# Performance work log

Hardware: AMD Instinct MI355X
Metric: run time of the kernel (lower is better)

Reference implementation:

```python
import jax, jax.numpy as jnp
import numpy as np

NUM_HEADS = 8
EMBED_CH = 512   # k channels
OUT_CH = 256     # v channels
MASK_CURRENT = False
NEG_INF = -1e30


def setup_inputs() -> dict:
    key = jax.random.key(0)
    ks = jax.random.split(key, 7)
    N, C, H, W = 8, 256, 32, 32
    s = lambda fan: 1.0 / np.sqrt(fan)
    return {
        "x": jax.random.normal(ks[0], (N, C, H, W), jnp.float32),
        "Wq": jax.random.normal(ks[1], (EMBED_CH, C), jnp.float32) * s(C),
        "bq": jax.random.normal(ks[2], (EMBED_CH,), jnp.float32) * 0.01,
        "Wkv": jax.random.normal(ks[3], (EMBED_CH + OUT_CH, C), jnp.float32) * s(C),
        "bkv": jax.random.normal(ks[4], (EMBED_CH + OUT_CH,), jnp.float32) * 0.01,
        "Wo": jax.random.normal(ks[5], (OUT_CH, OUT_CH), jnp.float32) * s(OUT_CH),
        "bo": jax.random.normal(ks[6], (OUT_CH,), jnp.float32) * 0.01,
    }


def _to_multihead(t, n, T):
    # t: [n, h*d, T] with channel layout '(h d)' -> [n, h, T, d]
    h = NUM_HEADS
    return t.reshape(n, h, -1, T).transpose(0, 1, 3, 2)


def reference(x, Wq, bq, Wkv, bkv, Wo, bo):
    n, C, H, W = x.shape
    T = H * W
    xf = x.reshape(n, C, T)  # flatten spatial dims into sequence

    # 1x1 convs == pointwise channel GEMMs
    q = jnp.einsum('oc,nct->not', Wq, xf) + bq[None, :, None]
    kv = jnp.einsum('oc,nct->not', Wkv, xf) + bkv[None, :, None]
    k, v = kv[:, :EMBED_CH], kv[:, EMBED_CH:]

    q = _to_multihead(q, n, T)   # [n, h, T, dk]
    k = _to_multihead(k, n, T)   # [n, h, T, dk]
    v = _to_multihead(v, n, T)   # [n, h, T, dv]

    dk = k.shape[-1]
    scale = 1.0 / np.sqrt(dk).astype(np.float32)

    # causal mask over flattened spatial positions (lower-triangular)
    diag = -1 if MASK_CURRENT else 0
    mask = jnp.tril(jnp.ones((T, T), dtype=bool), k=diag)  # [T, T]

    attn = jnp.einsum('nhtd,nhsd->nhts', q, k) * scale
    attn = jnp.where(mask[None, None], attn, NEG_INF)
    attn = jax.nn.softmax(attn, axis=-1)
    attn = jnp.where(mask[None, None], attn, 0.0)

    out = jnp.einsum('nhts,nhsd->nhtd', attn, v)            # [n, h, T, dv]
    out = out.transpose(0, 1, 3, 2).reshape(n, OUT_CH, T)   # n (h d) t

    out = jnp.einsum('oc,nct->not', Wo, out) + bo[None, :, None]
    return out.reshape(n, OUT_CH, H, W)
```

## Files before the change

kernel.cpp:

```cpp
#include <hip/hip_runtime.h>
#include <hip/hip_bf16.h>
#include <math.h>

typedef __bf16 bf16;
typedef __attribute__((ext_vector_type(4))) __bf16 bf16x4;
typedef __attribute__((ext_vector_type(8))) __bf16 bf16x8;
typedef __attribute__((ext_vector_type(4))) float f32x4;

#define T_DIM 1024
#define C_DIM 256
#define HEADS 8

static __device__ __forceinline__ int tb(int row, int col) {
  return row * 128 + ((((col >> 3) ^ row) & 7) << 4) + ((col & 7) << 1);
}

static __device__ __forceinline__ void gl16(const char* g, char* l) {
  __builtin_amdgcn_global_load_lds(
      (const __attribute__((address_space(1))) unsigned int*)g,
      (__attribute__((address_space(3))) unsigned int*)l, 16, 0, 0);
}
static __device__ __forceinline__ void stage16k(const char* g, char* l, int tid) {
  const int w = (tid >> 6) * 1024, ln = (tid & 63) * 16;
#pragma unroll
  for (int i = 0; i < 4; ++i) gl16(g + i * 4096 + w + ln, l + i * 4096 + w);
}
static __device__ __forceinline__ void stage8k(const char* g, char* l, int tid) {
  const int w = (tid >> 6) * 1024, ln = (tid & 63) * 16;
#pragma unroll
  for (int i = 0; i < 2; ++i) gl16(g + i * 4096 + w + ln, l + i * 4096 + w);
}
static __device__ __forceinline__ void stage4k(const char* g, char* l, int tid) {
  gl16(g + (tid >> 6) * 1024 + (tid & 63) * 16, l + (tid >> 6) * 1024);
}

__global__ __launch_bounds__(256) void k_prep(const float* __restrict__ x,
    const float* __restrict__ Wq, const float* __restrict__ Wkv, const float* __restrict__ Wo,
    char* __restrict__ xTt, char* __restrict__ Wbt, char* __restrict__ Wot) {
  const int tid = threadIdx.x;
  const int b = blockIdx.x;
  if (b < 512) {
    __shared__ float tile[64][65];
    const int n = b >> 6, rem = b & 63, tt64 = rem >> 2, ct = (rem & 3) << 6;
    const float* xp = x + ((size_t)n * C_DIM + ct) * T_DIM + tt64 * 64;
    const int t4 = (tid & 15) * 4, c0 = tid >> 4;
#pragma unroll
    for (int i = 0; i < 4; ++i) {
      const int c = c0 + i * 16;
      float4 v = *(const float4*)(xp + (size_t)c * T_DIM + t4);
      tile[c][t4] = v.x; tile[c][t4 + 1] = v.y; tile[c][t4 + 2] = v.z; tile[c][t4 + 3] = v.w;
    }
    __syncthreads();
    char* dst = xTt + (((size_t)(n * 8 + (tt64 >> 1))) * 4 + (rem & 3)) * 16384;
    const int rbase = (tt64 & 1) * 64;
#pragma unroll
    for (int i = 0; i < 2; ++i) {
      const int idx = tid + i * 256;
      const int tl = idx >> 3, c8 = (idx & 7) * 8;
      bf16x8 v;
#pragma unroll
      for (int j = 0; j < 8; ++j) v[j] = (bf16)tile[c8 + j][tl];
      *(bf16x8*)(dst + tb(rbase + tl, c8)) = v;
    }
  } else {
    const bool isWo = (b >= 532);
    const int o0 = (b - (isWo ? 532 : 512)) * 64;
#pragma unroll
    for (int i = 0; i < 8; ++i) {
      const int idx = tid + i * 256;
      const int row = idx >> 5, c8 = (idx & 31) * 8;
      const int o = o0 + row;
      const float* src = isWo ? (Wo + (size_t)o * C_DIM + c8)
                              : (o < 512 ? Wq + (size_t)o * C_DIM + c8
                                         : Wkv + (size_t)(o - 512) * C_DIM + c8);
      float4 a = *(const float4*)src;
      float4 bq4 = *(const float4*)(src + 4);
      bf16x8 v;
      v[0]=(bf16)a.x; v[1]=(bf16)a.y; v[2]=(bf16)a.z; v[3]=(bf16)a.w;
      v[4]=(bf16)bq4.x; v[5]=(bf16)bq4.y; v[6]=(bf16)bq4.z; v[7]=(bf16)bq4.w;
      char* base = isWo ? Wot : Wbt;
      char* dst = base + (((size_t)(o >> 7)) * 4 + (c8 >> 6)) * 16384;
      *(bf16x8*)(dst + tb(o & 127, c8 & 63)) = v;
    }
  }
}

__global__ __launch_bounds__(256) void k_qkv(const char* __restrict__ Wbt, const char* __restrict__ xTt,
    const float* __restrict__ bq, const float* __restrict__ bkv,
    bf16* __restrict__ q_ws, char* __restrict__ Kt, char* __restrict__ Vt) {
  __shared__ __attribute__((aligned(128))) unsigned char smem[34816];
  const int tid = threadIdx.x;
  const int nt = blockIdx.x, mt = blockIdx.y, n = blockIdx.z;
  const int w = tid >> 6, lane = tid & 63, lrow = lane & 15, lg = lane >> 4;
  const int wm = (w >> 1) * 64, wn = (w & 1) * 64;
  const char* gA = Wbt + (size_t)mt * 65536;
  const char* gB = xTt + ((size_t)(n * 8 + nt)) * 65536;

  f32x4 acc[4][4] = {};
#pragma unroll 1
  for (int kk = 0; kk < 4; ++kk) {
    stage16k(gA + kk * 16384, (char*)smem, tid);
    stage16k(gB + kk * 16384, (char*)smem + 16384, tid);
    __syncthreads();
    const char* As = (const char*)smem;
    const char* Bs = As + 16384;
    bf16x8 af[4][2], bv[4][2];
#pragma unroll
    for (int mi = 0; mi < 4; ++mi)
#pragma unroll
      for (int kh = 0; kh < 2; ++kh)
        af[mi][kh] = *(const bf16x8*)(As + tb(wm + mi * 16 + lrow, kh * 32 + lg * 8));
#pragma unroll
    for (int ni = 0; ni < 4; ++ni)
#pragma unroll
      for (int kh = 0; kh < 2; ++kh)
        bv[ni][kh] = *(const bf16x8*)(Bs + tb(wn + ni * 16 + lrow, kh * 32 + lg * 8));
#pragma unroll
    for (int kh = 0; kh < 2; ++kh)
#pragma unroll
      for (int mi = 0; mi < 4; ++mi)
#pragma unroll
        for (int ni = 0; ni < 4; ++ni)
          acc[mi][ni] = __builtin_amdgcn_mfma_f32_16x16x32_bf16(af[mi][kh], bv[ni][kh], acc[mi][ni], 0, 0, 0);
    __syncthreads();
  }

  const int obase = mt * 128 + wm + lg * 4;
  const int tcol0 = nt * 128 + wn + lrow;
  if (mt < 8) {
#pragma unroll
    for (int mi = 0; mi < 4; ++mi) {
      const int o = obase + mi * 16;
      if (mt < 4) {
        const float4 bb = *(const float4*)(bq + o);
        const int nh = n * 8 + (o >> 6), d = o & 63;
        bf16* qrow = q_ws + (size_t)nh * (T_DIM * 64) + d;
#pragma unroll
        for (int ni = 0; ni < 4; ++ni) {
          const int t = tcol0 + ni * 16;
          f32x4 v = acc[mi][ni];
          bf16x4 pk;
          pk[0]=(bf16)(v[0]+bb.x); pk[1]=(bf16)(v[1]+bb.y); pk[2]=(bf16)(v[2]+bb.z); pk[3]=(bf16)(v[3]+bb.w);
          *(bf16x4*)(qrow + (size_t)t * 64) = pk;
        }
      } else {
        const int o2 = o - 512;
        const float4 bb = *(const float4*)(bkv + o2);
        const int nh = n * 8 + (o2 >> 6), d = o2 & 63;
        char* tbase = Kt + (size_t)nh * 16 * 8192;
#pragma unroll
        for (int ni = 0; ni < 4; ++ni) {
          const int t = tcol0 + ni * 16;
          f32x4 v = acc[mi][ni];
          bf16x4 pk;
          pk[0]=(bf16)(v[0]+bb.x); pk[1]=(bf16)(v[1]+bb.y); pk[2]=(bf16)(v[2]+bb.z); pk[3]=(bf16)(v[3]+bb.w);
          *(bf16x4*)(tbase + (t >> 6) * 8192 + tb(t & 63, d)) = pk;
        }
      }
    }
  } else {
    bf16* tp = (bf16*)smem;
#pragma unroll
    for (int mi = 0; mi < 4; ++mi) {
      const int o3g = (mt - 8) * 128 + wm + mi * 16 + lg * 4;
      const float4 bb = *(const float4*)(bkv + 512 + o3g);
      const float* bbp = (const float*)&bb;
      const int o3l = wm + mi * 16 + lg * 4;
#pragma unroll
      for (int ni = 0; ni < 4; ++ni) {
        const int tl = wn + ni * 16 + lrow;
        f32x4 v = acc[mi][ni];
#pragma unroll
        for (int r = 0; r < 4; ++r)
          tp[(o3l + r) * 132 + tl] = (bf16)(v[r] + bbp[r]);
      }
    }
    __syncthreads();
    const int row = tid >> 1, half = tid & 1;
    const int o3 = (mt - 8) * 128 + row;
    const int nh = n * 8 + (o3 >> 5), dv = o3 & 31;
    char* tile = Vt + (size_t)nh * 16 * 4096 + (nt * 2 + half) * 4096;
    const bf16* src = tp + row * 132 + half * 64;
#pragma unroll
    for (int g = 0; g < 8; ++g) {
      bf16x4 lo = *(const bf16x4*)(src + g * 8);
      bf16x4 hi = *(const bf16x4*)(src + g * 8 + 4);
      bf16x8 vv;
      vv[0]=lo[0]; vv[1]=lo[1]; vv[2]=lo[2]; vv[3]=lo[3];
      vv[4]=hi[0]; vv[5]=hi[1]; vv[6]=hi[2]; vv[7]=hi[3];
      *(bf16x8*)(tile + tb(dv, g * 8)) = vv;
    }
  }
}

__global__ __launch_bounds__(256) void k_attn(const bf16* __restrict__ q_ws,
    const char* __restrict__ Kt, const char* __restrict__ Vt, char* __restrict__ attTt) {
  __shared__ __attribute__((aligned(128))) unsigned char smem[40960];
  const int tid = threadIdx.x;
  const int nh = blockIdx.x, qp = blockIdx.y;
  const int w = tid >> 6, lane = tid & 63, lrow = lane & 15, lg = lane >> 4;
  const int tl = w * 16 + lrow;
  const char* Ktb = Kt + (size_t)nh * 16 * 8192;
  const char* Vtb = Vt + (size_t)nh * 16 * 4096;
  const int n = nh >> 3, h = nh & 7;
  const float s2 = 0.18033688f;

  const int qt0 = qp, qt1 = 15 - qp;
  const int tg0 = qt0 * 64 + tl, tg1 = qt1 * 64 + tl;
  const bf16* qb0 = q_ws + ((size_t)nh * T_DIM + tg0) * 64;
  const bf16* qb1 = q_ws + ((size_t)nh * T_DIM + tg1) * 64;
  const bf16x8 qA0 = *(const bf16x8*)(qb0 + lg * 8);
  const bf16x8 qA1 = *(const bf16x8*)(qb0 + 32 + lg * 8);
  const bf16x8 qB0 = *(const bf16x8*)(qb1 + lg * 8);
  const bf16x8 qB1 = *(const bf16x8*)(qb1 + 32 + lg * 8);

  float m0 = -INFINITY, l0 = 0.f, m1 = -INFINITY, l1 = 0.f;
  f32x4 o0a = {}, o0b = {}, o1a = {}, o1b = {};

  auto proc = [&](bf16x8 qf0, bf16x8 qf1, float& m, float& l, f32x4& oa, f32x4& ob,
                  const char* Kbs, const char* Vbs, char* pws, bool diag) {
    f32x4 sacc[4];
    __builtin_amdgcn_s_setprio(1);
#pragma unroll
    for (int rt = 0; rt < 4; ++rt) {
      f32x4 a = {0.f, 0.f, 0.f, 0.f};
      bf16x8 kf0 = *(const bf16x8*)(Kbs + tb(rt * 16 + lrow, lg * 8));
      a = __builtin_amdgcn_mfma_f32_16x16x32_bf16(kf0, qf0, a, 0, 0, 0);
      bf16x8 kf1 = *(const bf16x8*)(Kbs + tb(rt * 16 + lrow, 32 + lg * 8));
      a = __builtin_amdgcn_mfma_f32_16x16x32_bf16(kf1, qf1, a, 0, 0, 0);
      sacc[rt] = a;
    }
    __builtin_amdgcn_s_setprio(0);
    float p[16];
#pragma unroll
    for (int rt = 0; rt < 4; ++rt)
#pragma unroll
      for (int r = 0; r < 4; ++r) {
        float v = sacc[rt][r] * s2;
        if (diag && (rt * 16 + lg * 4 + r) > tl) v = -INFINITY;
        p[rt * 4 + r] = v;
      }
    float pmax = p[0];
#pragma unroll
    for (int i = 1; i < 16; ++i) pmax = fmaxf(pmax, p[i]);
    pmax = fmaxf(pmax, __shfl_xor(pmax, 16));
    pmax = fmaxf(pmax, __shfl_xor(pmax, 32));
    const float mn = fmaxf(m, pmax);
    const float corr = exp2f(m - mn);
    float ps = 0.f;
#pragma unroll
    for (int i = 0; i < 16; ++i) { p[i] = exp2f(p[i] - mn); ps += p[i]; }
    ps += __shfl_xor(ps, 16);
    ps += __shfl_xor(ps, 32);
    l = l * corr + ps;
    m = mn;
    oa = oa * corr;
    ob = ob * corr;
#pragma unroll
    for (int rt = 0; rt < 4; ++rt) {
      bf16x4 pk;
#pragma unroll
      for (int r = 0; r < 4; ++r) pk[r] = (bf16)p[rt * 4 + r];
      *(bf16x4*)(pws + tb(lrow, rt * 16 + lg * 4)) = pk;
    }
    __builtin_amdgcn_s_setprio(1);
#pragma unroll
    for (int ks = 0; ks < 2; ++ks) {
      bf16x8 pf = *(const bf16x8*)(pws + tb(lrow, ks * 32 + lg * 8));
      bf16x8 vf0 = *(const bf16x8*)(Vbs + tb(lrow, ks * 32 + lg * 8));
      oa = __builtin_amdgcn_mfma_f32_16x16x32_bf16(vf0, pf, oa, 0, 0, 0);
      bf16x8 vf1 = *(const bf16x8*)(Vbs + tb(16 + lrow, ks * 32 + lg * 8));
      ob = __builtin_amdgcn_mfma_f32_16x16x32_bf16(vf1, pf, ob, 0, 0, 0);
    }
    __builtin_amdgcn_s_setprio(0);
  };

#pragma unroll 1
  for (int st2 = 0; st2 <= qt1; st2 += 2) {
    const bool has1 = (st2 + 1 <= qt1);
    stage8k(Ktb + (size_t)st2 * 8192, (char*)smem, tid);
    if (has1) stage8k(Ktb + (size_t)(st2 + 1) * 8192, (char*)smem + 8192, tid);
    stage4k(Vtb + (size_t)st2 * 4096, (char*)smem + 16384, tid);
    if (has1) stage4k(Vtb + (size_t)(st2 + 1) * 4096, (char*)smem + 20480, tid);
    __syncthreads();
    const int nsub = has1 ? 2 : 1;
#pragma unroll 1
    for (int sub = 0; sub < nsub; ++sub) {
      const int stk = st2 + sub;
      const char* Kbs = (const char*)smem + sub * 8192;
      const char* Vbs = (const char*)smem + 16384 + sub * 4096;
      char* pws = (char*)smem + 24576 + w * 4096 + sub * 2048;
      proc(qB0, qB1, m1, l1, o1a, o1b, Kbs, Vbs, pws, stk == qt1);
      if (stk <= qt0)
        proc(qA0, qA1, m0, l0, o0a, o0b, Kbs, Vbs, pws, stk == qt0);
    }
    __syncthreads();
  }

  auto epi = [&](int tg, float l, f32x4 oa, f32x4 ob) {
    const float inv = 1.0f / l;
    const int ntt = tg >> 7, row = tg & 127;
#pragma unroll
    for (int dt = 0; dt < 2; ++dt) {
      const f32x4 v = dt ? ob : oa;
      const int c = h * 32 + dt * 16 + lg * 4;
      char* tile = attTt + (((size_t)(n * 8 + ntt)) * 4 + (c >> 6)) * 16384;
      bf16x4 pk;
#pragma unroll
      for (int r = 0; r < 4; ++r) pk[r] = (bf16)(v[r] * inv);
      *(bf16x4*)(tile + tb(row, c & 63)) = pk;
    }
  };
  epi(tg0, l0, o0a, o0b);
  epi(tg1, l1, o1a, o1b);
}

__global__ __launch_bounds__(256) void k_proj(const char* __restrict__ attTt,
    const char* __restrict__ Wot, const float* __restrict__ bo, float* __restrict__ out) {
  __shared__ __attribute__((aligned(128))) unsigned char smem[16384];
  const int tid = threadIdx.x;
  const int tm = blockIdx.x, om = blockIdx.y, n = blockIdx.z;
  const int w = tid >> 6, lane = tid & 63, lrow = lane & 15, lg = lane >> 4;
  const int wm = (w >> 1) * 32, wn = (w & 1) * 32;
  const char* gA = attTt + ((size_t)(n * 8 + (tm >> 1))) * 65536 + (tm & 1) * 8192;
  const char* gB = Wot + (size_t)(om >> 1) * 65536 + (om & 1) * 8192;

  f32x4 acc[2][2] = {};
#pragma unroll 1
  for (int kk = 0; kk < 4; ++kk) {
    stage8k(gA + kk * 16384, (char*)smem, tid);
    stage8k(gB + kk * 16384, (char*)smem + 8192, tid);
    __syncthreads();
    const char* As = (const char*)smem;
    const char* Bs = As + 8192;
    bf16x8 af[2][2], bv[2][2];
#pragma unroll
    for (int mi = 0; mi < 2; ++mi)
#pragma unroll
      for (int kh = 0; kh < 2; ++kh)
        af[mi][kh] = *(const bf16x8*)(As + tb(wm + mi * 16 + lrow, kh * 32 + lg * 8));
#pragma unroll
    for (int ni = 0; ni < 2; ++ni)
#pragma unroll
      for (int kh = 0; kh < 2; ++kh)
        bv[ni][kh] = *(const bf16x8*)(Bs + tb(wn + ni * 16 + lrow, kh * 32 + lg * 8));
#pragma unroll
    for (int kh = 0; kh < 2; ++kh)
#pragma unroll
      for (int mi = 0; mi < 2; ++mi)
#pragma unroll
        for (int ni = 0; ni < 2; ++ni)
          acc[mi][ni] = __builtin_amdgcn_mfma_f32_16x16x32_bf16(af[mi][kh], bv[ni][kh], acc[mi][ni], 0, 0, 0);
    __syncthreads();
  }

  const int t0b = tm * 64 + wm + lg * 4;
  const int ob = om * 64 + wn + lrow;
#pragma unroll
  for (int mi = 0; mi < 2; ++mi) {
    const int t0 = t0b + mi * 16;
#pragma unroll
    for (int ni = 0; ni < 2; ++ni) {
      const int o = ob + ni * 16;
      const float bb = bo[o];
      f32x4 v = acc[mi][ni];
      v[0] += bb; v[1] += bb; v[2] += bb; v[3] += bb;
      *(f32x4*)(out + ((size_t)(n * C_DIM + o)) * T_DIM + t0) = v;
    }
  }
}

extern "C" void kernel_launch(void* const* d_in, const int* in_sizes, int n_in,
                              void* d_out, int out_size, void* d_ws, size_t ws_size,
                              hipStream_t stream) {
  const float* x   = (const float*)d_in[0];
  const float* Wq  = (const float*)d_in[1];
  const float* bq  = (const float*)d_in[2];
  const float* Wkv = (const float*)d_in[3];
  const float* bkv = (const float*)d_in[4];
  const float* Wo  = (const float*)d_in[5];
  const float* bo  = (const float*)d_in[6];
  float* out = (float*)d_out;

  char* ws = (char*)d_ws;
  char* xTt   = ws;
  char* Wbt   = ws + (4u  << 20);
  char* Wot   = ws + (5u  << 20);
  bf16* q_ws  = (bf16*)(ws + (6u << 20));
  char* Kt    = ws + (14u << 20);
  char* Vt    = ws + (22u << 20);
  char* attTt = ws + (26u << 20);

  k_prep<<<536, 256, 0, stream>>>(x, Wq, Wkv, Wo, xTt, Wbt, Wot);
  k_qkv<<<dim3(8, 10, 8), 256, 0, stream>>>(Wbt, xTt, bq, bkv, q_ws, Kt, Vt);
  k_attn<<<dim3(64, 8), 256, 0, stream>>>(q_ws, Kt, Vt, attTt);
  k_proj<<<dim3(16, 4, 8), 256, 0, stream>>>(attTt, Wot, bo, out);
}
```

Before: 59.58 us.

## Fuse four kernels into one cooperative persistent kernel with grid syncs

Replaces the four separate launches (prep, qkv, attention, projection) with a single cooperative kernel of 512 blocks. Grid-wide barriers separate the stages, and each stage's work is mapped onto block indices, with 128 blocks taking a second qkv tile. This is meant to remove inter-kernel launch gaps and tail drain. The cost is grid-sync overhead, load imbalance in the qkv stage, and a two-blocks-per-CU occupancy constraint enforced by the launch bounds.

```diff
diff --git a/kernel.cpp b/kernel.cpp
--- a/kernel.cpp
+++ b/kernel.cpp
@@ -1,6 +1,9 @@
 #include <hip/hip_runtime.h>
 #include <hip/hip_bf16.h>
+#include <hip/hip_cooperative_groups.h>
 #include <math.h>
+
+namespace cg = cooperative_groups;
 
 typedef __bf16 bf16;
 typedef __attribute__((ext_vector_type(4))) __bf16 bf16x4;
@@ -34,63 +37,64 @@
   gl16(g + (tid >> 6) * 1024 + (tid & 63) * 16, l + (tid >> 6) * 1024);
 }
 
-__global__ __launch_bounds__(256) void k_prep(const float* __restrict__ x,
-    const float* __restrict__ Wq, const float* __restrict__ Wkv, const float* __restrict__ Wo,
-    char* __restrict__ xTt, char* __restrict__ Wbt, char* __restrict__ Wot) {
-  const int tid = threadIdx.x;
-  const int b = blockIdx.x;
-  if (b < 512) {
-    __shared__ float tile[64][65];
-    const int n = b >> 6, rem = b & 63, tt64 = rem >> 2, ct = (rem & 3) << 6;
-    const float* xp = x + ((size_t)n * C_DIM + ct) * T_DIM + tt64 * 64;
-    const int t4 = (tid & 15) * 4, c0 = tid >> 4;
-#pragma unroll
-    for (int i = 0; i < 4; ++i) {
-      const int c = c0 + i * 16;
-      float4 v = *(const float4*)(xp + (size_t)c * T_DIM + t4);
-      tile[c][t4] = v.x; tile[c][t4 + 1] = v.y; tile[c][t4 + 2] = v.z; tile[c][t4 + 3] = v.w;
-    }
-    __syncthreads();
-    char* dst = xTt + (((size_t)(n * 8 + (tt64 >> 1))) * 4 + (rem & 3)) * 16384;
-    const int rbase = (tt64 & 1) * 64;
-#pragma unroll
-    for (int i = 0; i < 2; ++i) {
-      const int idx = tid + i * 256;
-      const int tl = idx >> 3, c8 = (idx & 7) * 8;
-      bf16x8 v;
-#pragma unroll
-      for (int j = 0; j < 8; ++j) v[j] = (bf16)tile[c8 + j][tl];
-      *(bf16x8*)(dst + tb(rbase + tl, c8)) = v;
-    }
-  } else {
-    const bool isWo = (b >= 532);
-    const int o0 = (b - (isWo ? 532 : 512)) * 64;
-#pragma unroll
-    for (int i = 0; i < 8; ++i) {
-      const int idx = tid + i * 256;
-      const int row = idx >> 5, c8 = (idx & 31) * 8;
-      const int o = o0 + row;
-      const float* src = isWo ? (Wo + (size_t)o * C_DIM + c8)
-                              : (o < 512 ? Wq + (size_t)o * C_DIM + c8
-                                         : Wkv + (size_t)(o - 512) * C_DIM + c8);
-      float4 a = *(const float4*)src;
-      float4 bq4 = *(const float4*)(src + 4);
-      bf16x8 v;
-      v[0]=(bf16)a.x; v[1]=(bf16)a.y; v[2]=(bf16)a.z; v[3]=(bf16)a.w;
-      v[4]=(bf16)bq4.x; v[5]=(bf16)bq4.y; v[6]=(bf16)bq4.z; v[7]=(bf16)bq4.w;
-      char* base = isWo ? Wot : Wbt;
-      char* dst = base + (((size_t)(o >> 7)) * 4 + (c8 >> 6)) * 16384;
-      *(bf16x8*)(dst + tb(o & 127, c8 & 63)) = v;
-    }
-  }
-}
-
-__global__ __launch_bounds__(256) void k_qkv(const char* __restrict__ Wbt, const char* __restrict__ xTt,
-    const float* __restrict__ bq, const float* __restrict__ bkv,
-    bf16* __restrict__ q_ws, char* __restrict__ Kt, char* __restrict__ Vt) {
-  __shared__ __attribute__((aligned(128))) unsigned char smem[34816];
-  const int tid = threadIdx.x;
-  const int nt = blockIdx.x, mt = blockIdx.y, n = blockIdx.z;
+static __device__ __forceinline__ void prep_transpose(int b, const float* __restrict__ x,
+    char* __restrict__ xTt, unsigned char* smem, int tid) {
+  float (*tile)[65] = (float (*)[65])smem;
+  const int n = b >> 6, rem = b & 63, tt64 = rem >> 2, ct = (rem & 3) << 6;
+  const float* xp = x + ((size_t)n * C_DIM + ct) * T_DIM + tt64 * 64;
+  const int t4 = (tid & 15) * 4, c0 = tid >> 4;
+#pragma unroll
+  for (int i = 0; i < 4; ++i) {
+    const int c = c0 + i * 16;
+    float4 v = *(const float4*)(xp + (size_t)c * T_DIM + t4);
+    tile[c][t4] = v.x; tile[c][t4 + 1] = v.y; tile[c][t4 + 2] = v.z; tile[c][t4 + 3] = v.w;
+  }
+  __syncthreads();
+  char* dst = xTt + (((size_t)(n * 8 + (tt64 >> 1))) * 4 + (rem & 3)) * 16384;
+  const int rbase = (tt64 & 1) * 64;
+#pragma unroll
+  for (int i = 0; i < 2; ++i) {
+    const int idx = tid + i * 256;
+    const int tl = idx >> 3, c8 = (idx & 7) * 8;
+    bf16x8 v;
+#pragma unroll
+    for (int j = 0; j < 8; ++j) v[j] = (bf16)tile[c8 + j][tl];
+    *(bf16x8*)(dst + tb(rbase + tl, c8)) = v;
+  }
+}
+
+static __device__ __forceinline__ void prep_w(int u, const float* __restrict__ Wq,
+    const float* __restrict__ Wkv, const float* __restrict__ Wo,
+    char* __restrict__ Wbt, char* __restrict__ Wot, int tid) {
+  const bool isWo = (u >= 20);
+  const int o0 = (isWo ? (u - 20) : u) * 64;
+#pragma unroll
+  for (int i = 0; i < 8; ++i) {
+    const int idx = tid + i * 256;
+    const int row = idx >> 5, c8 = (idx & 31) * 8;
+    const int o = o0 + row;
+    const float* src = isWo ? (Wo + (size_t)o * C_DIM + c8)
+                            : (o < 512 ? Wq + (size_t)o * C_DIM + c8
+                                       : Wkv + (size_t)(o - 512) * C_DIM + c8);
+    float4 a = *(const float4*)src;
+    float4 bq4 = *(const float4*)(src + 4);
+    bf16x8 v;
+    v[0]=(bf16)a.x; v[1]=(bf16)a.y; v[2]=(bf16)a.z; v[3]=(bf16)a.w;
+    v[4]=(bf16)bq4.x; v[5]=(bf16)bq4.y; v[6]=(bf16)bq4.z; v[7]=(bf16)bq4.w;
+    char* base = isWo ? Wot : Wbt;
+    char* dst = base + (((size_t)(o >> 7)) * 4 + (c8 >> 6)) * 16384;
+    *(bf16x8*)(dst + tb(o & 127, c8 & 63)) = v;
+  }
+}
+
+static __device__ __forceinline__ void qkv_job(int j, const char* __restrict__ Wbt,
+    const char* __restrict__ xTt, const float* __restrict__ bq, const float* __restrict__ bkv,
+    bf16* __restrict__ q_ws, char* __restrict__ Kt, char* __restrict__ Vt,
+    unsigned char* smem, int tid) {
+  const int nt = j & 7;
+  const int mtn = j >> 3;
+  const int n = mtn / 10;
+  const int mt = mtn - n * 10;
   const int w = tid >> 6, lane = tid & 63, lrow = lane & 15, lg = lane >> 4;
   const int wm = (w >> 1) * 64, wn = (w & 1) * 64;
   const char* gA = Wbt + (size_t)mt * 65536;
@@ -193,11 +197,10 @@
   }
 }
 
-__global__ __launch_bounds__(256) void k_attn(const bf16* __restrict__ q_ws,
-    const char* __restrict__ Kt, const char* __restrict__ Vt, char* __restrict__ attTt) {
-  __shared__ __attribute__((aligned(128))) unsigned char smem[40960];
-  const int tid = threadIdx.x;
-  const int nh = blockIdx.x, qp = blockIdx.y;
+static __device__ __forceinline__ void attn_job(int bj, const bf16* __restrict__ q_ws,
+    const char* __restrict__ Kt, const char* __restrict__ Vt, char* __restrict__ attTt,
+    unsigned char* smem, int tid) {
+  const int nh = bj & 63, qp = bj >> 6;
   const int w = tid >> 6, lane = tid & 63, lrow = lane & 15, lg = lane >> 4;
   const int tl = w * 16 + lrow;
   const char* Ktb = Kt + (size_t)nh * 16 * 8192;
@@ -315,11 +318,10 @@
   epi(tg1, l1, o1a, o1b);
 }
 
-__global__ __launch_bounds__(256) void k_proj(const char* __restrict__ attTt,
-    const char* __restrict__ Wot, const float* __restrict__ bo, float* __restrict__ out) {
-  __shared__ __attribute__((aligned(128))) unsigned char smem[16384];
-  const int tid = threadIdx.x;
-  const int tm = blockIdx.x, om = blockIdx.y, n = blockIdx.z;
+static __device__ __forceinline__ void proj_job(int bj, const char* __restrict__ attTt,
+    const char* __restrict__ Wot, const float* __restrict__ bo, float* __restrict__ out,
+    unsigned char* smem, int tid) {
+  const int tm = bj & 15, om = (bj >> 4) & 3, n = bj >> 6;
   const int w = tid >> 6, lane = tid & 63, lrow = lane & 15, lg = lane >> 4;
   const int wm = (w >> 1) * 32, wn = (w & 1) * 32;
   const char* gA = attTt + ((size_t)(n * 8 + (tm >> 1))) * 65536 + (tm & 1) * 8192;
@@ -368,6 +370,35 @@
       *(f32x4*)(out + ((size_t)(n * C_DIM + o)) * T_DIM + t0) = v;
     }
   }
+}
+
+__global__ __launch_bounds__(256, 2) void k_fused(const float* __restrict__ x,
+    const float* __restrict__ Wq, const float* __restrict__ bq,
+    const float* __restrict__ Wkv, const float* __restrict__ bkv,
+    const float* __restrict__ Wo, const float* __restrict__ bo, float* __restrict__ out,
+    char* __restrict__ xTt, char* __restrict__ Wbt, char* __restrict__ Wot,
+    bf16* __restrict__ q_ws, char* __restrict__ Kt, char* __restrict__ Vt,
+    char* __restrict__ attTt) {
+  cg::grid_group grid = cg::this_grid();
+  __shared__ __attribute__((aligned(128))) unsigned char smem[40960];
+  const int tid = threadIdx.x;
+  const int b = blockIdx.x;
+
+  prep_transpose(b, x, xTt, smem, tid);
+  if (b >= 488) prep_w(b - 488, Wq, Wkv, Wo, Wbt, Wot, tid);
+  grid.sync();
+
+  qkv_job(b, Wbt, xTt, bq, bkv, q_ws, Kt, Vt, smem, tid);
+  if (b < 128) {
+    __syncthreads();
+    qkv_job(512 + b, Wbt, xTt, bq, bkv, q_ws, Kt, Vt, smem, tid);
+  }
+  grid.sync();
+
+  attn_job(b, q_ws, Kt, Vt, attTt, smem, tid);
+  grid.sync();
+
+  proj_job(b, attTt, Wot, bo, out, smem, tid);
 }
 
 extern "C" void kernel_launch(void* const* d_in, const int* in_sizes, int n_in,
@@ -391,8 +422,8 @@
   char* Vt    = ws + (22u << 20);
   char* attTt = ws + (26u << 20);
 
-  k_prep<<<536, 256, 0, stream>>>(x, Wq, Wkv, Wo, xTt, Wbt, Wot);
-  k_qkv<<<dim3(8, 10, 8), 256, 0, stream>>>(Wbt, xTt, bq, bkv, q_ws, Kt, Vt);
-  k_attn<<<dim3(64, 8), 256, 0, stream>>>(q_ws, Kt, Vt, attTt);
-  k_proj<<<dim3(16, 4, 8), 256, 0, stream>>>(attTt, Wot, bo, out);
-}
+  void* args[] = { &x, &Wq, &bq, &Wkv, &bkv, &Wo, &bo, &out,
+                   &xTt, &Wbt, &Wot, &q_ws, &Kt, &Vt, &attTt };
+  hipLaunchCooperativeKernel((const void*)k_fused, dim3(512), dim3(256),
+                             args, 0, stream);
+}
```

Result: slower. 236.8 us (+297.5%).
